# Performance work log

Hardware: AMD Instinct MI355X
Metric: run time of the kernel (lower is better)

Reference implementation:

```python
import jax, jax.numpy as jnp
import numpy as np

B, P, K, E, H, V, C = 128, 64, 64, 300, 300, 50000, 3


def lstm0(x, Wih, bih, bhh):
    # PyTorch LSTMCell single step with zero initial (h, c) state.
    # gates = x @ Wih^T + bih + Whh @ 0 + bhh ; chunks order: i, f, g, o
    g = x @ Wih.T + bih + bhh
    i, f, gg, o = jnp.split(g, 4, axis=-1)
    c = jax.nn.sigmoid(i) * jnp.tanh(gg)
    return jax.nn.sigmoid(o) * jnp.tanh(c)


def setup_inputs() -> dict:
    key = jax.random.key(0)
    ks = jax.random.split(key, 24)
    d = {}
    d["premise"] = jax.random.randint(ks[0], (B, P), 1, V)
    d["premise_len"] = jax.random.randint(ks[1], (B,), P // 2, P + 1)
    d["hypothesis"] = jax.random.randint(ks[2], (B, K), 1, V)
    d["hypothesis_len"] = jax.random.randint(ks[3], (B,), K // 2, K + 1)
    embed = jax.random.normal(ks[4], (V, E), jnp.float32) * 0.1
    d["embed"] = embed.at[0].set(0.0)  # padding_idx=0
    d["w_e"] = jax.random.uniform(ks[5], (H,), jnp.float32)
    xav = (2.0 / (H + H)) ** 0.5
    d["W_s"] = jax.random.normal(ks[6], (H, H), jnp.float32) * xav
    d["W_t"] = jax.random.normal(ks[7], (H, H), jnp.float32) * xav
    d["W_m"] = jax.random.normal(ks[8], (H, H), jnp.float32) * xav
    d["fc_w"] = jax.random.normal(ks[9], (C, H), jnp.float32) * (2.0 / (H + C)) ** 0.5
    d["fc_b"] = jax.random.uniform(ks[10], (C,), jnp.float32)
    s = 1.0 / np.sqrt(H)
    def cell(k1, k2, k3, k4, in_dim):
        return (jax.random.uniform(k1, (4 * H, in_dim), jnp.float32, -s, s),
                jax.random.uniform(k2, (4 * H, H), jnp.float32, -s, s),
                jax.random.uniform(k3, (4 * H,), jnp.float32, -s, s),
                jax.random.uniform(k4, (4 * H,), jnp.float32, -s, s))
    d["Wih_p"], d["Whh_p"], d["bih_p"], d["bhh_p"] = cell(ks[11], ks[12], ks[13], ks[14], E)
    d["Wih_h"], d["Whh_h"], d["bih_h"], d["bhh_h"] = cell(ks[15], ks[16], ks[17], ks[18], E)
    d["Wih_m"], d["Whh_m"], d["bih_m"], d["bhh_m"] = cell(ks[19], ks[20], ks[21], ks[22], 2 * H)
    return d


def reference(premise, premise_len, hypothesis, hypothesis_len, embed, w_e,
              W_s, W_t, W_m, fc_w, fc_b,
              Wih_p, Whh_p, bih_p, bhh_p,
              Wih_h, Whh_h, bih_h, bhh_h,
              Wih_m, Whh_m, bih_m, bhh_m):
    prem_emb = embed[premise]      # [B,P,E]
    hypo_emb = embed[hypothesis]   # [B,K,E]
    # Original code calls LSTMCell on a whole sequence -> per-token single step
    # with zero initial state (no temporal recurrence in these two cells).
    h_s = lstm0(prem_emb, Wih_p, bih_p, bhh_p)  # [B,P,H]
    h_t = lstm0(hypo_emb, Wih_h, bih_h, bhh_h)  # [B,K,H]
    s_proj = h_s @ W_s.T                         # [B,P,H]
    t_proj = jnp.transpose(h_t @ W_t.T, (1, 0, 2))  # [K,B,H]
    h_t_kb = jnp.transpose(h_t, (1, 0, 2))          # [K,B,H]
    b, p = h_s.shape[0], h_s.shape[1]
    pmask = jnp.arange(p)[None, :] < premise_len[:, None]  # [B,P]
    neg = jnp.finfo(s_proj.dtype).min

    def step(h_m, xs):
        t_k, ht_k = xs  # [B,H], [B,H]
        m_proj = h_m @ W_m.T  # [B,H]
        e = jnp.einsum('bph,h->bp',
                       jnp.tanh(s_proj + t_k[:, None, :] + m_proj[:, None, :]), w_e)
        e = jnp.where(pmask, e, neg)
        alpha = jax.nn.softmax(e, axis=1)           # softmax over valid premise pos
        a = jnp.einsum('bp,bph->bh', alpha, h_s)    # attention-weighted premise
        m = jnp.concatenate([a, ht_k], axis=-1)     # [B,2H]
        # lstm_match is re-invoked with zero state each k in the original
        h_m_new = lstm0(m, Wih_m, bih_m, bhh_m)
        return h_m_new, h_m_new

    _, hs_all = jax.lax.scan(step, jnp.zeros((b, s_proj.shape[-1]), s_proj.dtype),
                             (t_proj, h_t_kb))      # [K,B,H]
    h_fin = hs_all[hypothesis_len - 1, jnp.arange(b)]  # h_m at last valid hypo step
    logits = h_fin @ fc_w.T + fc_b
    return jax.nn.softmax(logits, axis=1)
```

## Files before the change

kernel.cpp:

```cpp
#include <hip/hip_runtime.h>
#include <stdint.h>

typedef unsigned short u16;
typedef __attribute__((ext_vector_type(8))) __bf16 bf16x8;
typedef __attribute__((ext_vector_type(4))) float f32x4;

__device__ __forceinline__ float bf2f(u16 u) {
    union { unsigned int i; float f; } v; v.i = ((unsigned int)u) << 16; return v.f;
}
__device__ __forceinline__ float bf2f_lo(unsigned int u) {
    union { unsigned int i; float f; } v; v.i = u << 16; return v.f;
}
__device__ __forceinline__ float bf2f_hi(unsigned int u) {
    union { unsigned int i; float f; } v; v.i = u & 0xffff0000u; return v.f;
}
__device__ __forceinline__ u16 f2bf(float f) {
    union { float f; unsigned int i; } v; v.f = f;
    unsigned int x = v.i;
    unsigned int r = (x + 0x7fffu + ((x >> 16) & 1u)) >> 16;
    return (u16)r;
}
__device__ __forceinline__ float rdf(const void* p, size_t i, int isbf) {
    return isbf ? bf2f(((const u16*)p)[i]) : ((const float*)p)[i];
}
__device__ __forceinline__ float fast_sigmoid(float x) {
    return __builtin_amdgcn_rcpf(1.f + __expf(-x));
}
__device__ __forceinline__ float fast_tanh(float x) {
    float u = __expf(x + x);
    return 1.f - 2.f * __builtin_amdgcn_rcpf(u + 1.f);
}
__device__ __forceinline__ bf16x8 as_bf8(uint4 u) {
    union { uint4 a; bf16x8 b; } c; c.a = u; return c.b;
}

#define BB 128
#define PP 64
#define KK 64
#define HH 300
#define MROWS 8192
#define KPAD 320
#define N3H 900
#define GLD 912
#define NT1 19
#define NT4 57

__global__ void detect_dtype(const u16* __restrict__ raw, int* __restrict__ flag) {
    __shared__ int cnt;
    if (threadIdx.x == 0) cnt = 0;
    __syncthreads();
    if (threadIdx.x < 300 && (raw[threadIdx.x] & 0x8000u)) atomicAdd(&cnt, 1);
    __syncthreads();
    if (threadIdx.x == 0) *flag = (cnt < 8) ? 1 : 0;
}

__global__ void pack_w(const void* __restrict__ src, u16* __restrict__ dst,
                       int dstRowsPad, int nsrcRows, int srcld, int colOff, int igo,
                       const int* __restrict__ flag) {
    int i = blockIdx.x * 256 + threadIdx.x;
    if (i >= dstRowsPad * KPAD) return;
    int isbf = *flag;
    int r = i / KPAD, c = i % KPAD;
    u16 v = 0;
    if (r < nsrcRows && c < HH) {
        int sr = igo ? (r < HH ? r : r + HH) : r;
        v = f2bf(rdf(src, (size_t)sr * srcld + colOff + c, isbf));
    }
    dst[i] = v;
}

__global__ void pack_wf(const void* __restrict__ Wm, uint4* __restrict__ dst,
                        const int* __restrict__ flag) {
    int i = blockIdx.x * 256 + threadIdx.x;
    if (i >= NT1 * 10 * 64) return;
    int isbf = *flag;
    int lane = i & 63, ks = (i >> 6) % 10, T = i / 640;
    int j = T * 16 + (lane & 15);
    int k0 = 32 * ks + 8 * (lane >> 4);
    unsigned int d[4];
    #pragma unroll
    for (int q = 0; q < 4; ++q) {
        int ka = k0 + 2 * q, kb = k0 + 2 * q + 1;
        unsigned int lo = (j < 300 && ka < 300) ? f2bf(rdf(Wm, (size_t)j * HH + ka, isbf)) : 0;
        unsigned int hi = (j < 300 && kb < 300) ? f2bf(rdf(Wm, (size_t)j * HH + kb, isbf)) : 0;
        d[q] = lo | (hi << 16);
    }
    uint4 v; v.x = d[0]; v.y = d[1]; v.z = d[2]; v.w = d[3];
    dst[i] = v;
}

__global__ void pack_bias(const void* bip, const void* bhp, const void* bih_, const void* bhh_,
                          const void* bim, const void* bhm,
                          float* bp, float* bh, float* bm, const int* __restrict__ flag) {
    int i = blockIdx.x * 256 + threadIdx.x;
    if (i >= 3 * N3H) return;
    int isbf = *flag;
    int which = i / N3H, r = i % N3H;
    int sr = (r < HH) ? r : r + HH;
    if (which == 0)      bp[r] = rdf(bip, sr, isbf) + rdf(bhp, sr, isbf);
    else if (which == 1) bh[r] = rdf(bih_, sr, isbf) + rdf(bhh_, sr, isbf);
    else                 bm[r] = rdf(bim, sr, isbf) + rdf(bhm, sr, isbf);
}

__global__ void gather_embed(const int* __restrict__ idx, const void* __restrict__ embed,
                             u16* __restrict__ X, const int* __restrict__ flag) {
    int i = blockIdx.x * 256 + threadIdx.x;
    int isbf = *flag;
    int r = i / KPAD, c = i % KPAD;
    X[i] = (c < HH) ? f2bf(rdf(embed, (size_t)idx[r] * HH + c, isbf)) : (u16)0;
}

__global__ void zero_out(u16* out) { out[threadIdx.x] = 0; }

__global__ __launch_bounds__(256) void gemm_bt(
    const u16* __restrict__ A, const u16* __restrict__ B,
    u16* __restrict__ Cb, const float* __restrict__ bias, int N, int ldc, int frag)
{
    __shared__ __align__(16) u16 At[128 * 32];
    __shared__ __align__(16) u16 Bt[128 * 32];
    const int tid = threadIdx.x;
    const int m0 = blockIdx.x * 128;
    const int n0 = blockIdx.y * 128;
    const int lane = tid & 63;
    const int wave = tid >> 6;
    const int rm = (wave & 1) * 64;
    const int rn = (wave >> 1) * 64;
    const int qr = lane >> 4;
    const int lr = lane & 15;

    f32x4 acc[4][4] = {};

    const int c0 = tid, c1 = tid + 256;
    const int r0 = c0 >> 2, o0 = (c0 & 3) * 8;
    const int r1 = c1 >> 2, o1 = (c1 & 3) * 8;

    for (int k0 = 0; k0 < KPAD; k0 += 32) {
        uint4 a0v = *(const uint4*)(A + (size_t)(m0 + r0) * KPAD + k0 + o0);
        uint4 a1v = *(const uint4*)(A + (size_t)(m0 + r1) * KPAD + k0 + o1);
        uint4 b0v = *(const uint4*)(B + (size_t)(n0 + r0) * KPAD + k0 + o0);
        uint4 b1v = *(const uint4*)(B + (size_t)(n0 + r1) * KPAD + k0 + o1);
        __syncthreads();
        *(uint4*)(At + c0 * 8) = a0v;
        *(uint4*)(At + c1 * 8) = a1v;
        *(uint4*)(Bt + c0 * 8) = b0v;
        *(uint4*)(Bt + c1 * 8) = b1v;
        __syncthreads();
        bf16x8 af[4], bfr[4];
        #pragma unroll
        for (int i = 0; i < 4; ++i) {
            af[i]  = *(const bf16x8*)(At + (rm + i * 16 + lr) * 32 + qr * 8);
            bfr[i] = *(const bf16x8*)(Bt + (rn + i * 16 + lr) * 32 + qr * 8);
        }
        #pragma unroll
        for (int mi = 0; mi < 4; ++mi)
            #pragma unroll
            for (int ni = 0; ni < 4; ++ni)
                acc[mi][ni] = __builtin_amdgcn_mfma_f32_16x16x32_bf16(
                    af[mi], bfr[ni], acc[mi][ni], 0, 0, 0);
    }
    #pragma unroll
    for (int mi = 0; mi < 4; ++mi) {
        #pragma unroll
        for (int ni = 0; ni < 4; ++ni) {
            int n = n0 + rn + ni * 16 + lr;
            int mb = m0 + rm + mi * 16 + qr * 4;
            if (!frag) {
                if (n >= ldc) continue;
                if (n < N) {
                    float bv = bias ? bias[n] : 0.f;
                    #pragma unroll
                    for (int r = 0; r < 4; ++r)
                        Cb[(size_t)(mb + r) * ldc + n] = f2bf(acc[mi][ni][r] + bv);
                } else {
                    #pragma unroll
                    for (int r = 0; r < 4; ++r)
                        Cb[(size_t)(mb + r) * ldc + n] = 0;
                }
            } else {
                if (n >= GLD) continue;
                int bb = mb >> 6, p0 = mb & 63;
                size_t base = ((((size_t)bb * NT4 + (n >> 4)) * 2 + (p0 >> 5)) * 64
                               + ((p0 >> 3) & 3) * 16 + (n & 15)) * 8 + (p0 & 7);
                u16 wv[4];
                if (n < N) {
                    float bv = bias ? bias[n] : 0.f;
                    #pragma unroll
                    for (int r = 0; r < 4; ++r) wv[r] = f2bf(acc[mi][ni][r] + bv);
                } else {
                    #pragma unroll
                    for (int r = 0; r < 4; ++r) wv[r] = 0;
                }
                uint2 st;
                st.x = (unsigned int)wv[0] | ((unsigned int)wv[1] << 16);
                st.y = (unsigned int)wv[2] | ((unsigned int)wv[3] << 16);
                *(uint2*)(Cb + base) = st;
            }
        }
    }
}

__global__ void lstm_act(const u16* __restrict__ gates, u16* __restrict__ hout) {
    int idx = blockIdx.x * 256 + threadIdx.x;
    int r = idx / KPAD, c = idx % KPAD;
    float h = 0.f;
    if (c < HH) {
        const u16* g = gates + (size_t)r * N3H;
        float gi = bf2f(g[c]);
        float gg = bf2f(g[c + HH]);
        float go = bf2f(g[c + 2 * HH]);
        float cc = fast_sigmoid(gi) * fast_tanh(gg);
        h = fast_sigmoid(go) * fast_tanh(cc);
    }
    hout[idx] = f2bf(h);
}

__global__ __launch_bounds__(512, 2) void scan_kernel(
    const u16* __restrict__ sproj,
    const u16* __restrict__ tproj,
    const uint4* __restrict__ Gmf,
    const u16* __restrict__ hp,
    const uint4* __restrict__ Wf,
    const void* __restrict__ w_e,
    const int* __restrict__ premise_len,
    const int* __restrict__ hypothesis_len,
    float* __restrict__ hfin,
    const int* __restrict__ flag)
{
    __shared__ __align__(16) uint4 gml[NT4 * 2 * 64];
    __shared__ __align__(16) float we2[320];
    __shared__ __align__(16) float tpm[304];
    __shared__ __align__(16) unsigned int hmhi[160];
    __shared__ __align__(16) unsigned int hmlo[160];
    __shared__ __align__(16) u16 ahi[64];
    __shared__ __align__(16) u16 alo[64];
    __shared__ float evals[64];
    __shared__ __align__(16) float gates[912];

    const int b = blockIdx.x, t = threadIdx.x;
    const int lane = t & 63, w = t >> 6;
    const int lr = lane & 15, qr = lane >> 4;
    const int plen = premise_len[b], hlen = hypothesis_len[b];
    const int isbf = *flag;

    {
        const uint4* gsrc = Gmf + (size_t)b * (NT4 * 2 * 64);
        for (int i = t; i < NT4 * 2 * 64; i += 512) gml[i] = gsrc[i];
    }
    if (t < 320) we2[t] = (t < 300) ? 2.f * rdf(w_e, t, isbf) : 0.f;
    if (t < 160) { hmhi[t] = 0; hmlo[t] = 0; }
    __syncthreads();

    const int p2p = t >> 3, p2s = t & 7;
    unsigned int spd[19];
    {
        const unsigned int* sprow = (const unsigned int*)(sproj + (size_t)(b * PP + p2p) * KPAD);
        #pragma unroll
        for (int i = 0; i < 19; ++i) spd[i] = sprow[p2s + 8 * i];
    }
    float wsum = 0.f;
    #pragma unroll
    for (int i = 0; i < 19; ++i) {
        float2 wv = ((const float2*)we2)[p2s + 8 * i];
        wsum += 0.5f * (wv.x + wv.y);
    }

    const int nt4 = (w == 0) ? 8 : 7;

    for (int k = 0; k < hlen; ++k) {
        const u16* tprow = tproj + (size_t)(b * KK + k) * KPAD;
        const u16* hprow = hp + (size_t)(b * KK + k) * 900;

        u16 hpv[8];
        #pragma unroll
        for (int i = 0; i < 8; ++i) {
            hpv[i] = 0;
            if (i < nt4 && lane < 16) hpv[i] = hprow[(w + 8 * i) * 16 + lane];
        }
        u16 tk0 = 0, tk1 = 0, tk2 = 0;
        if (lane < 16) {
            tk0 = tprow[w * 16 + lane];
            tk1 = tprow[(w + 8) * 16 + lane];
            if (w < 3) tk2 = tprow[(w + 16) * 16 + lane];
        }

        uint4 bA[10], bB[10];
        #pragma unroll
        for (int ks = 0; ks < 10; ++ks) bA[ks] = Wf[(size_t)w * 640 + ks * 64 + lane];
        #pragma unroll
        for (int ks = 0; ks < 10; ++ks) bB[ks] = Wf[(size_t)(w + 8) * 640 + ks * 64 + lane];

        bf16x8 a1[10];
        {
            const unsigned int* abase = (lr == 1) ? hmlo : hmhi;
            uint4 z; z.x = 0; z.y = 0; z.z = 0; z.w = 0;
            #pragma unroll
            for (int ks = 0; ks < 10; ++ks) {
                uint4 u = *(const uint4*)(abase + 16 * ks + 4 * qr);
                a1[ks] = as_bf8((lr < 2) ? u : z);
            }
        }
        {
            f32x4 acc = {};
            #pragma unroll
            for (int ks = 0; ks < 10; ++ks)
                acc = __builtin_amdgcn_mfma_f32_16x16x32_bf16(a1[ks], as_bf8(bA[ks]), acc, 0, 0, 0);
            if (lane < 16) tpm[w * 16 + lane] = 2.f * (bf2f(tk0) + acc[0] + acc[1]);
        }
        if (w < 3) {
            #pragma unroll
            for (int ks = 0; ks < 10; ++ks) bA[ks] = Wf[(size_t)(w + 16) * 640 + ks * 64 + lane];
        }
        {
            f32x4 acc = {};
            #pragma unroll
            for (int ks = 0; ks < 10; ++ks)
                acc = __builtin_amdgcn_mfma_f32_16x16x32_bf16(a1[ks], as_bf8(bB[ks]), acc, 0, 0, 0);
            if (lane < 16) tpm[(w + 8) * 16 + lane] = 2.f * (bf2f(tk1) + acc[0] + acc[1]);
        }
        if (w < 3) {
            f32x4 acc = {};
            #pragma unroll
            for (int ks = 0; ks < 10; ++ks)
                acc = __builtin_amdgcn_mfma_f32_16x16x32_bf16(a1[ks], as_bf8(bA[ks]), acc, 0, 0, 0);
            if (lane < 16) tpm[(w + 16) * 16 + lane] = 2.f * (bf2f(tk2) + acc[0] + acc[1]);
        }
        __syncthreads();

        {
            float accn = 0.f;
            bool act = p2p < plen;
            if (act) {
                #pragma unroll
                for (int i = 0; i < 19; ++i) {
                    unsigned int spv = spd[i];
                    float2 tv = ((const float2*)tpm)[p2s + 8 * i];
                    float2 wv = ((const float2*)we2)[p2s + 8 * i];
                    float x0 = fmaf(2.f, bf2f_lo(spv), tv.x);
                    float x1 = fmaf(2.f, bf2f_hi(spv), tv.y);
                    accn = fmaf(wv.x, __builtin_amdgcn_rcpf(__expf(x0) + 1.f), accn);
                    accn = fmaf(wv.y, __builtin_amdgcn_rcpf(__expf(x1) + 1.f), accn);
                }
            }
            float val = act ? (wsum - accn) : 0.f;
            val += __shfl_down(val, 4);
            val += __shfl_down(val, 2);
            val += __shfl_down(val, 1);
            if (p2s == 0) evals[p2p] = act ? val : -1e30f;
        }
        __syncthreads();

        if (w == 0) {
            float v = evals[lane];
            float mx = v;
            #pragma unroll
            for (int d = 32; d; d >>= 1) mx = fmaxf(mx, __shfl_xor(mx, d));
            float ex = (lane < plen) ? __expf(v - mx) : 0.f;
            float sm = ex;
            #pragma unroll
            for (int d = 32; d; d >>= 1) sm += __shfl_xor(sm, d);
            float al = ex * __builtin_amdgcn_rcpf(sm);
            u16 ah = f2bf(al);
            ahi[lane] = ah;
            alo[lane] = f2bf(al - bf2f(ah));
        }
        __syncthreads();

        bf16x8 a4[2];
        {
            const u16* abase = (lr == 1) ? alo : ahi;
            uint4 z; z.x = 0; z.y = 0; z.z = 0; z.w = 0;
            #pragma unroll
            for (int ks = 0; ks < 2; ++ks) {
                uint4 u = *(const uint4*)(abase + 32 * ks + 8 * qr);
                a4[ks] = as_bf8((lr < 2) ? u : z);
            }
        }
        #pragma unroll
        for (int i = 0; i < 8; ++i) {
            if (i < nt4) {
                int T = w + 8 * i;
                bf16x8 g0 = as_bf8(gml[(T * 2 + 0) * 64 + lane]);
                bf16x8 g1 = as_bf8(gml[(T * 2 + 1) * 64 + lane]);
                f32x4 acc = {};
                acc = __builtin_amdgcn_mfma_f32_16x16x32_bf16(a4[0], g0, acc, 0, 0, 0);
                acc = __builtin_amdgcn_mfma_f32_16x16x32_bf16(a4[1], g1, acc, 0, 0, 0);
                if (lane < 16) gates[T * 16 + lane] = acc[0] + acc[1] + bf2f(hpv[i]);
            }
        }
        __syncthreads();

        if (t < 300) {
            float gi = gates[t], gg = gates[300 + t], go = gates[600 + t];
            float cc = fast_sigmoid(gi) * fast_tanh(gg);
            float h = fast_sigmoid(go) * fast_tanh(cc);
            if (k == hlen - 1) hfin[(size_t)b * KPAD + t] = h;
            u16 hh = f2bf(h);
            float res = h - bf2f(hh);
            float hn = __shfl_down(h, 1);
            float rn2 = __shfl_down(res, 1);
            if ((t & 1) == 0) {
                hmhi[t >> 1] = (unsigned int)hh | ((unsigned int)f2bf(hn) << 16);
                hmlo[t >> 1] = (unsigned int)f2bf(res) | ((unsigned int)f2bf(rn2) << 16);
            }
        }
        __syncthreads();
    }
}

__global__ void fc_softmax(const float* __restrict__ hfin, const void* __restrict__ fcw,
                           const void* __restrict__ fcb, void* __restrict__ out,
                           const int* __restrict__ flag) {
    int b = threadIdx.x;
    int isbf = *flag;
    float l[3];
    #pragma unroll
    for (int c = 0; c < 3; ++c) {
        float acc = rdf(fcb, c, isbf);
        const float* hr = hfin + (size_t)b * KPAD;
        for (int h = 0; h < HH; ++h) acc += hr[h] * rdf(fcw, (size_t)c * HH + h, isbf);
        l[c] = acc;
    }
    float mx = fmaxf(l[0], fmaxf(l[1], l[2]));
    float e0 = __expf(l[0] - mx), e1 = __expf(l[1] - mx), e2 = __expf(l[2] - mx);
    float inv = __builtin_amdgcn_rcpf(e0 + e1 + e2);
    if (isbf) {
        u16* o = (u16*)out;
        o[b * 3 + 0] = f2bf(e0 * inv);
        o[b * 3 + 1] = f2bf(e1 * inv);
        o[b * 3 + 2] = f2bf(e2 * inv);
    } else {
        float* o = (float*)out;
        o[b * 3 + 0] = e0 * inv;
        o[b * 3 + 1] = e1 * inv;
        o[b * 3 + 2] = e2 * inv;
    }
}

extern "C" void kernel_launch(void* const* d_in, const int* in_sizes, int n_in,
                              void* d_out, int out_size, void* d_ws, size_t ws_size,
                              hipStream_t stream) {
    const int* premise        = (const int*)d_in[0];
    const int* premise_len    = (const int*)d_in[1];
    const int* hypothesis     = (const int*)d_in[2];
    const int* hypothesis_len = (const int*)d_in[3];
    const void* embed = d_in[4];
    const void* w_e   = d_in[5];
    const void* W_s   = d_in[6];
    const void* W_t   = d_in[7];
    const void* W_m   = d_in[8];
    const void* fc_w  = d_in[9];
    const void* fc_b  = d_in[10];
    const void* Wih_p = d_in[11];
    const void* bih_p = d_in[13];
    const void* bhh_p = d_in[14];
    const void* Wih_h = d_in[15];
    const void* bih_h = d_in[17];
    const void* bhh_h = d_in[18];
    const void* Wih_m = d_in[19];
    const void* bih_m = d_in[21];
    const void* bhh_m = d_in[22];
    (void)in_sizes; (void)n_in; (void)out_size;

    char* w = (char*)d_ws;
    auto alloc = [&](size_t bytes) -> char* {
        char* r = (char*)(((uintptr_t)w + 255) & ~(uintptr_t)255);
        w = r + bytes;
        return r;
    };
    char* regA = alloc((size_t)MROWS * KPAD * 2);
    char* regB = alloc((size_t)MROWS * GLD * 2);
    char* regC = alloc((size_t)MROWS * N3H * 2);
    char* regD = alloc((size_t)MROWS * KPAD * 2);
    char* regE = alloc((size_t)MROWS * KPAD * 2);
    u16* Wp_pad  = (u16*)alloc((size_t)1024 * KPAD * 2);
    u16* Wh_pad  = (u16*)alloc((size_t)1024 * KPAD * 2);
    u16* Wa_pad  = (u16*)alloc((size_t)1024 * KPAD * 2);
    u16* Whm_pad = (u16*)alloc((size_t)1024 * KPAD * 2);
    u16* Ws_pad  = (u16*)alloc((size_t)384 * KPAD * 2);
    u16* Wt_pad  = (u16*)alloc((size_t)384 * KPAD * 2);
    uint4* Wf    = (uint4*)alloc((size_t)NT1 * 10 * 64 * 16);
    float* bsum_p = (float*)alloc(N3H * 4);
    float* bsum_h = (float*)alloc(N3H * 4);
    float* bsum_m = (float*)alloc(N3H * 4);
    int* dflag   = (int*)alloc(256);
    size_t needed = (size_t)(w - (char*)d_ws);
    if (needed > ws_size) {
        zero_out<<<1, 384, 0, stream>>>((u16*)d_out);
        return;
    }
    u16* Xbuf   = (u16*)regA;
    u16* s_proj = (u16*)regA;
    u16* h_s    = (u16*)regD;
    u16* t_proj = (u16*)regD;
    u16* h_t    = (u16*)regE;
    float* h_fin = (float*)regE;

    detect_dtype<<<1, 320, 0, stream>>>((const u16*)w_e, dflag);
    pack_w<<<1280, 256, 0, stream>>>(Wih_p, Wp_pad, 1024, N3H, HH, 0, 1, dflag);
    pack_w<<<1280, 256, 0, stream>>>(Wih_h, Wh_pad, 1024, N3H, HH, 0, 1, dflag);
    pack_w<<<1280, 256, 0, stream>>>(Wih_m, Wa_pad, 1024, N3H, 600, 0, 1, dflag);
    pack_w<<<1280, 256, 0, stream>>>(Wih_m, Whm_pad, 1024, N3H, 600, HH, 1, dflag);
    pack_w<<<480, 256, 0, stream>>>(W_s, Ws_pad, 384, HH, HH, 0, 0, dflag);
    pack_w<<<480, 256, 0, stream>>>(W_t, Wt_pad, 384, HH, HH, 0, 0, dflag);
    pack_wf<<<48, 256, 0, stream>>>(W_m, Wf, dflag);
    pack_bias<<<11, 256, 0, stream>>>(bih_p, bhh_p, bih_h, bhh_h, bih_m, bhh_m,
                                      bsum_p, bsum_h, bsum_m, dflag);

    gather_embed<<<10240, 256, 0, stream>>>(premise, embed, Xbuf, dflag);
    gemm_bt<<<dim3(64, 8), 256, 0, stream>>>(Xbuf, Wp_pad, (u16*)regB, bsum_p, N3H, N3H, 0);
    lstm_act<<<10240, 256, 0, stream>>>((u16*)regB, h_s);
    gather_embed<<<10240, 256, 0, stream>>>(hypothesis, embed, Xbuf, dflag);
    gemm_bt<<<dim3(64, 8), 256, 0, stream>>>(Xbuf, Wh_pad, (u16*)regC, bsum_h, N3H, N3H, 0);
    lstm_act<<<10240, 256, 0, stream>>>((u16*)regC, h_t);

    gemm_bt<<<dim3(64, 3), 256, 0, stream>>>(h_s, Ws_pad, s_proj, nullptr, HH, KPAD, 0);
    gemm_bt<<<dim3(64, 8), 256, 0, stream>>>(h_s, Wa_pad, (u16*)regB, nullptr, N3H, 0, 1);
    gemm_bt<<<dim3(64, 3), 256, 0, stream>>>(h_t, Wt_pad, t_proj, nullptr, HH, KPAD, 0);
    gemm_bt<<<dim3(64, 8), 256, 0, stream>>>(h_t, Whm_pad, (u16*)regC, bsum_m, N3H, N3H, 0);

    scan_kernel<<<BB, 512, 0, stream>>>(s_proj, t_proj, (const uint4*)regB,
                                        (const u16*)regC, Wf, w_e,
                                        premise_len, hypothesis_len, h_fin, dflag);
    fc_softmax<<<1, 128, 0, stream>>>(h_fin, fc_w, fc_b, d_out, dflag);
}
```

Baseline: 694.2 us.

## Keep recurrent W_m and attention weights resident in registers across scan steps

```diff
diff --git a/kernel.cpp b/kernel.cpp
--- a/kernel.cpp
+++ b/kernel.cpp
@@ -214,7 +214,7 @@
     hout[idx] = f2bf(h);
 }
 
-__global__ __launch_bounds__(512, 2) void scan_kernel(
+__global__ __launch_bounds__(512, 1) void scan_kernel(
     const u16* __restrict__ sproj,
     const u16* __restrict__ tproj,
     const uint4* __restrict__ Gmf,
@@ -226,13 +226,12 @@
     float* __restrict__ hfin,
     const int* __restrict__ flag)
 {
-    __shared__ __align__(16) uint4 gml[NT4 * 2 * 64];
+    __shared__ __align__(16) uint4 wlds[3 * 10 * 64];
     __shared__ __align__(16) float we2[320];
-    __shared__ __align__(16) float tpm[304];
+    __shared__ __align__(16) float tpm[320];
     __shared__ __align__(16) unsigned int hmhi[160];
     __shared__ __align__(16) unsigned int hmlo[160];
-    __shared__ __align__(16) u16 ahi[64];
-    __shared__ __align__(16) u16 alo[64];
+    __shared__ __align__(16) u16 aw[8][128];
     __shared__ float evals[64];
     __shared__ __align__(16) float gates[912];
 
@@ -242,29 +241,48 @@
     const int plen = premise_len[b], hlen = hypothesis_len[b];
     const int isbf = *flag;
 
+    for (int i = t; i < 3 * 10 * 64; i += 512) wlds[i] = Wf[16 * 640 + i];
+    if (t < 320) { we2[t] = (t < 300) ? 2.f * rdf(w_e, t, isbf) : 0.f; tpm[t] = 0.f; }
+    if (t < 160) { hmhi[t] = 0; hmlo[t] = 0; }
+
+    uint4 wreg[20];
+    #pragma unroll
+    for (int ks = 0; ks < 10; ++ks) wreg[ks]      = Wf[(size_t)w * 640 + ks * 64 + lane];
+    #pragma unroll
+    for (int ks = 0; ks < 10; ++ks) wreg[10 + ks] = Wf[(size_t)(w + 8) * 640 + ks * 64 + lane];
+
+    const int nt4 = (w == 0) ? 8 : 7;
+    uint4 greg[16];
     {
         const uint4* gsrc = Gmf + (size_t)b * (NT4 * 2 * 64);
-        for (int i = t; i < NT4 * 2 * 64; i += 512) gml[i] = gsrc[i];
-    }
-    if (t < 320) we2[t] = (t < 300) ? 2.f * rdf(w_e, t, isbf) : 0.f;
-    if (t < 160) { hmhi[t] = 0; hmlo[t] = 0; }
+        #pragma unroll
+        for (int i = 0; i < 8; ++i) {
+            if (i < nt4) {
+                int T = w + 8 * i;
+                greg[2 * i]     = gsrc[(T * 2 + 0) * 64 + lane];
+                greg[2 * i + 1] = gsrc[(T * 2 + 1) * 64 + lane];
+            }
+        }
+    }
+
+    const int p2p = t >> 3, p2s = t & 7;
+    unsigned int spd[20];
+    {
+        const uint4* sprow = (const uint4*)(sproj + (size_t)(b * PP + p2p) * KPAD + 40 * p2s);
+        #pragma unroll
+        for (int q = 0; q < 5; ++q) {
+            uint4 v = sprow[q];
+            spd[4 * q] = v.x; spd[4 * q + 1] = v.y; spd[4 * q + 2] = v.z; spd[4 * q + 3] = v.w;
+        }
+    }
     __syncthreads();
 
-    const int p2p = t >> 3, p2s = t & 7;
-    unsigned int spd[19];
-    {
-        const unsigned int* sprow = (const unsigned int*)(sproj + (size_t)(b * PP + p2p) * KPAD);
-        #pragma unroll
-        for (int i = 0; i < 19; ++i) spd[i] = sprow[p2s + 8 * i];
-    }
     float wsum = 0.f;
     #pragma unroll
-    for (int i = 0; i < 19; ++i) {
-        float2 wv = ((const float2*)we2)[p2s + 8 * i];
-        wsum += 0.5f * (wv.x + wv.y);
-    }
-
-    const int nt4 = (w == 0) ? 8 : 7;
+    for (int q = 0; q < 10; ++q) {
+        float4 v = ((const float4*)we2)[10 * p2s + q];
+        wsum += 0.5f * ((v.x + v.y) + (v.z + v.w));
+    }
 
     for (int k = 0; k < hlen; ++k) {
         const u16* tprow = tproj + (size_t)(b * KK + k) * KPAD;
@@ -283,12 +301,6 @@
             if (w < 3) tk2 = tprow[(w + 16) * 16 + lane];
         }
 
-        uint4 bA[10], bB[10];
-        #pragma unroll
-        for (int ks = 0; ks < 10; ++ks) bA[ks] = Wf[(size_t)w * 640 + ks * 64 + lane];
-        #pragma unroll
-        for (int ks = 0; ks < 10; ++ks) bB[ks] = Wf[(size_t)(w + 8) * 640 + ks * 64 + lane];
-
         bf16x8 a1[10];
         {
             const unsigned int* abase = (lr == 1) ? hmlo : hmhi;
@@ -300,29 +312,33 @@
             }
         }
         {
-            f32x4 acc = {};
-            #pragma unroll
-            for (int ks = 0; ks < 10; ++ks)
-                acc = __builtin_amdgcn_mfma_f32_16x16x32_bf16(a1[ks], as_bf8(bA[ks]), acc, 0, 0, 0);
-            if (lane < 16) tpm[w * 16 + lane] = 2.f * (bf2f(tk0) + acc[0] + acc[1]);
+            f32x4 ac0 = {}, ac1 = {};
+            #pragma unroll
+            for (int ks = 0; ks < 10; ks += 2) {
+                ac0 = __builtin_amdgcn_mfma_f32_16x16x32_bf16(a1[ks], as_bf8(wreg[ks]), ac0, 0, 0, 0);
+                ac1 = __builtin_amdgcn_mfma_f32_16x16x32_bf16(a1[ks + 1], as_bf8(wreg[ks + 1]), ac1, 0, 0, 0);
+            }
+            if (lane < 16) tpm[w * 16 + lane] = 2.f * (bf2f(tk0) + ((ac0[0] + ac0[1]) + (ac1[0] + ac1[1])));
+        }
+        {
+            f32x4 ac0 = {}, ac1 = {};
+            #pragma unroll
+            for (int ks = 0; ks < 10; ks += 2) {
+                ac0 = __builtin_amdgcn_mfma_f32_16x16x32_bf16(a1[ks], as_bf8(wreg[10 + ks]), ac0, 0, 0, 0);
+                ac1 = __builtin_amdgcn_mfma_f32_16x16x32_bf16(a1[ks + 1], as_bf8(wreg[11 + ks]), ac1, 0, 0, 0);
+            }
+            if (lane < 16) tpm[(w + 8) * 16 + lane] = 2.f * (bf2f(tk1) + ((ac0[0] + ac0[1]) + (ac1[0] + ac1[1])));
         }
         if (w < 3) {
-            #pragma unroll
-            for (int ks = 0; ks < 10; ++ks) bA[ks] = Wf[(size_t)(w + 16) * 640 + ks * 64 + lane];
-        }
-        {
-            f32x4 acc = {};
-            #pragma unroll
-            for (int ks = 0; ks < 10; ++ks)
-                acc = __builtin_amdgcn_mfma_f32_16x16x32_bf16(a1[ks], as_bf8(bB[ks]), acc, 0, 0, 0);
-            if (lane < 16) tpm[(w + 8) * 16 + lane] = 2.f * (bf2f(tk1) + acc[0] + acc[1]);
-        }
-        if (w < 3) {
-            f32x4 acc = {};
-            #pragma unroll
-            for (int ks = 0; ks < 10; ++ks)
-                acc = __builtin_amdgcn_mfma_f32_16x16x32_bf16(a1[ks], as_bf8(bA[ks]), acc, 0, 0, 0);
-            if (lane < 16) tpm[(w + 16) * 16 + lane] = 2.f * (bf2f(tk2) + acc[0] + acc[1]);
+            f32x4 ac0 = {}, ac1 = {};
+            #pragma unroll
+            for (int ks = 0; ks < 10; ks += 2) {
+                bf16x8 b0 = as_bf8(wlds[w * 640 + ks * 64 + lane]);
+                bf16x8 b1 = as_bf8(wlds[w * 640 + (ks + 1) * 64 + lane]);
+                ac0 = __builtin_amdgcn_mfma_f32_16x16x32_bf16(a1[ks], b0, ac0, 0, 0, 0);
+                ac1 = __builtin_amdgcn_mfma_f32_16x16x32_bf16(a1[ks + 1], b1, ac1, 0, 0, 0);
+            }
+            if (lane < 16) tpm[(w + 16) * 16 + lane] = 2.f * (bf2f(tk2) + ((ac0[0] + ac0[1]) + (ac1[0] + ac1[1])));
         }
         __syncthreads();
 
@@ -331,14 +347,17 @@
             bool act = p2p < plen;
             if (act) {
                 #pragma unroll
-                for (int i = 0; i < 19; ++i) {
-                    unsigned int spv = spd[i];
-                    float2 tv = ((const float2*)tpm)[p2s + 8 * i];
-                    float2 wv = ((const float2*)we2)[p2s + 8 * i];
-                    float x0 = fmaf(2.f, bf2f_lo(spv), tv.x);
-                    float x1 = fmaf(2.f, bf2f_hi(spv), tv.y);
+                for (int q = 0; q < 10; ++q) {
+                    float4 tv = ((const float4*)tpm)[10 * p2s + q];
+                    float4 wv = ((const float4*)we2)[10 * p2s + q];
+                    float x0 = fmaf(2.f, bf2f_lo(spd[2 * q]), tv.x);
+                    float x1 = fmaf(2.f, bf2f_hi(spd[2 * q]), tv.y);
+                    float x2 = fmaf(2.f, bf2f_lo(spd[2 * q + 1]), tv.z);
+                    float x3 = fmaf(2.f, bf2f_hi(spd[2 * q + 1]), tv.w);
                     accn = fmaf(wv.x, __builtin_amdgcn_rcpf(__expf(x0) + 1.f), accn);
                     accn = fmaf(wv.y, __builtin_amdgcn_rcpf(__expf(x1) + 1.f), accn);
+                    accn = fmaf(wv.z, __builtin_amdgcn_rcpf(__expf(x2) + 1.f), accn);
+                    accn = fmaf(wv.w, __builtin_amdgcn_rcpf(__expf(x3) + 1.f), accn);
                 }
             }
             float val = act ? (wsum - accn) : 0.f;
@@ -349,7 +368,7 @@
         }
         __syncthreads();
 
-        if (w == 0) {
+        {
             float v = evals[lane];
             float mx = v;
             #pragma unroll
@@ -360,14 +379,13 @@
             for (int d = 32; d; d >>= 1) sm += __shfl_xor(sm, d);
             float al = ex * __builtin_amdgcn_rcpf(sm);
             u16 ah = f2bf(al);
-            ahi[lane] = ah;
-            alo[lane] = f2bf(al - bf2f(ah));
-        }
-        __syncthreads();
+            aw[w][lane] = ah;
+            aw[w][64 + lane] = f2bf(al - bf2f(ah));
+        }
 
         bf16x8 a4[2];
         {
-            const u16* abase = (lr == 1) ? alo : ahi;
+            const u16* abase = aw[w] + ((lr == 1) ? 64 : 0);
             uint4 z; z.x = 0; z.y = 0; z.z = 0; z.w = 0;
             #pragma unroll
             for (int ks = 0; ks < 2; ++ks) {
@@ -379,12 +397,10 @@
         for (int i = 0; i < 8; ++i) {
             if (i < nt4) {
                 int T = w + 8 * i;
-                bf16x8 g0 = as_bf8(gml[(T * 2 + 0) * 64 + lane]);
-                bf16x8 g1 = as_bf8(gml[(T * 2 + 1) * 64 + lane]);
-                f32x4 acc = {};
-                acc = __builtin_amdgcn_mfma_f32_16x16x32_bf16(a4[0], g0, acc, 0, 0, 0);
-                acc = __builtin_amdgcn_mfma_f32_16x16x32_bf16(a4[1], g1, acc, 0, 0, 0);
-                if (lane < 16) gates[T * 16 + lane] = acc[0] + acc[1] + bf2f(hpv[i]);
+                f32x4 ac0 = {}, ac1 = {};
+                ac0 = __builtin_amdgcn_mfma_f32_16x16x32_bf16(a4[0], as_bf8(greg[2 * i]), ac0, 0, 0, 0);
+                ac1 = __builtin_amdgcn_mfma_f32_16x16x32_bf16(a4[1], as_bf8(greg[2 * i + 1]), ac1, 0, 0, 0);
+                if (lane < 16) gates[T * 16 + lane] = ((ac0[0] + ac0[1]) + (ac1[0] + ac1[1])) + bf2f(hpv[i]);
             }
         }
         __syncthreads();
```

Result: no change. 688.8 us (-0.8%).
